# Kernel tuning notes

Hardware: AMD Instinct MI355X
Metric: run time of the kernel (lower is better)

## Reference

```python
import jax, jax.numpy as jnp
from jax import lax
import numpy as np

B, N, C = 16, 4096, 81          # batch, rois, classes (incl. background)
VARIANCES = np.array([0.1, 0.1, 0.2, 0.2], dtype=np.float32)
MAX_TOTAL = 200                  # max_total_size (= per-class cap here)
K = 200                          # per-class candidates kept before NMS
SCORE_TH = 0.5
IOU_TH = 0.5                     # tf combined NMS default
EPS = 1e-8


def setup_inputs() -> dict:
    key = jax.random.key(0)
    k1, k2, k3, k4 = jax.random.split(key, 4)
    yx = jax.random.uniform(k1, (B, N, 2)) * 0.8
    hw = 0.05 + jax.random.uniform(k2, (B, N, 2)) * 0.15
    roi_bboxes = jnp.concatenate([yx, yx + hw], axis=-1)          # [B,N,4] y1x1y2x2 in [0,1]
    pred_deltas = jax.random.normal(k3, (B, N, C * 4)) * 0.5      # [B,N,C*4]
    logits = jax.random.normal(k4, (B, N, C)) * 3.0
    pred_label_probs = jax.nn.softmax(logits, axis=-1)            # [B,N,C]
    return {"roi_bboxes": roi_bboxes, "pred_deltas": pred_deltas,
            "pred_label_probs": pred_label_probs}


def delta_to_bbox(anchors, deltas):
    # anchors [...,4] y1,x1,y2,x2 ; deltas [...,4] dy,dx,dh,dw
    ah = anchors[..., 2] - anchors[..., 0]
    aw = anchors[..., 3] - anchors[..., 1]
    acy = anchors[..., 0] + 0.5 * ah
    acx = anchors[..., 1] + 0.5 * aw
    bh = jnp.exp(deltas[..., 2]) * ah
    bw = jnp.exp(deltas[..., 3]) * aw
    bcy = deltas[..., 0] * ah + acy
    bcx = deltas[..., 1] * aw + acx
    y1 = bcy - 0.5 * bh
    x1 = bcx - 0.5 * bw
    return jnp.stack([y1, x1, y1 + bh, x1 + bw], axis=-1)


def pairwise_iou(boxes):  # [K,4] -> [K,K]
    y1 = jnp.maximum(boxes[:, None, 0], boxes[None, :, 0])
    x1 = jnp.maximum(boxes[:, None, 1], boxes[None, :, 1])
    y2 = jnp.minimum(boxes[:, None, 2], boxes[None, :, 2])
    x2 = jnp.minimum(boxes[:, None, 3], boxes[None, :, 3])
    inter = jnp.maximum(y2 - y1, 0.0) * jnp.maximum(x2 - x1, 0.0)
    area = jnp.maximum(boxes[:, 2] - boxes[:, 0], 0.0) * jnp.maximum(boxes[:, 3] - boxes[:, 1], 0.0)
    union = area[:, None] + area[None, :] - inter
    return inter / (union + EPS)


def _nms_keep(boxes_k, scores_k):
    # boxes_k [K,4] sorted by score desc; greedy suppression mask
    ious = pairwise_iou(boxes_k)
    rng = jnp.arange(K)
    valid = scores_k > SCORE_TH

    def step(keep, i):
        sup = (ious[i] > IOU_TH) & (rng > i) & keep[i]
        return keep & ~sup, None

    keep, _ = lax.scan(step, valid, rng)
    return keep


def _per_class(boxes_c, scores_c):
    # boxes_c [N,4], scores_c [N] -> top-K candidates + NMS-kept scores
    sc, idx = lax.top_k(scores_c, K)
    bx = boxes_c[idx]                       # [K,4]
    keep = _nms_keep(bx, sc)
    return bx, jnp.where(keep, sc, 0.0)


def _per_image(boxes_b, scores_b):
    # boxes_b [N,C,4], scores_b [N,C]
    bx, sc = jax.vmap(_per_class, in_axes=(1, 1))(boxes_b, scores_b)  # [C,K,4],[C,K]
    top_sc, top_idx = lax.top_k(sc.reshape(-1), MAX_TOTAL)
    top_bx = bx.reshape(-1, 4)[top_idx]
    top_lbl = (top_idx // K).astype(jnp.float32)
    valid = top_sc > 0.0
    top_bx = jnp.clip(jnp.where(valid[:, None], top_bx, 0.0), 0.0, 1.0)  # clip_boxes=True
    return top_bx, jnp.where(valid, top_sc, 0.0), jnp.where(valid, top_lbl, 0.0)


def reference(roi_bboxes, pred_deltas, pred_label_probs):
    b, n, _ = roi_bboxes.shape
    c = pred_label_probs.shape[-1]
    deltas = pred_deltas.reshape(b, n, c, 4) * jnp.asarray(VARIANCES)
    pred_bboxes = delta_to_bbox(roi_bboxes[:, :, None, :], deltas)       # [B,N,C,4]
    bg = jnp.argmax(pred_label_probs, axis=-1) == 0                      # background mask
    scores = jnp.where(bg[..., None], 0.0, pred_label_probs)             # [B,N,C]
    final_bboxes, final_scores, final_labels = jax.vmap(_per_image)(pred_bboxes, scores)
    return final_bboxes, final_labels, final_scores
```

## Files before the change

### kernel.cpp

```cpp
#include <hip/hip_runtime.h>
#include <math.h>

#pragma clang fp contract(off)

constexpr int NB  = 16;
constexpr int NR  = 4096;
constexpr int NC  = 81;
constexpr int NCM1 = NC - 1;
constexpr int KK  = 200;
constexpr int CAP = 4096;
constexpr int MAXC = 1024;
constexpr int TCHUNK = 256;
constexpr int NCHUNK = CAP / TCHUNK;
constexpr float SCORE_TH = 0.5f;
constexpr float IOU_TH   = 0.5f;
constexpr float EPSF     = 1e-8f;

struct SK { float s; int key; };

__global__ void k_perclass(const float* __restrict__ probs,
                           const float* __restrict__ roi,
                           const float* __restrict__ deltas,
                           int* __restrict__ kcnt,
                           SK* __restrict__ sk_seg,
                           float4* __restrict__ fbox_seg) {
    __shared__ int   lcnt;
    __shared__ float ls[MAXC], lroi[MAXC];
    __shared__ float ss[KK], sy1[KK], sx1[KK], sy2[KK], sx2[KK], sar[KK];
    __shared__ unsigned long long sup[KK][4];
    __shared__ int   skeep[KK];

    const int bid = blockIdx.x, tid = threadIdx.x;
    const int b = bid / NCM1, cm1 = bid % NCM1, c = cm1 + 1;

    if (tid == 0) lcnt = 0;
    __syncthreads();

    const float* pcol = probs + (size_t)b * NR * NC + c;
    #pragma unroll 4
    for (int r = tid; r < NR; r += 256) {
        float p = pcol[(size_t)r * NC];
        if (p > SCORE_TH) {
            int q = atomicAdd(&lcnt, 1);
            if (q < MAXC) { ls[q] = p; lroi[q] = (float)r; }
        }
    }
    __syncthreads();

    int Mc = lcnt < MAXC ? lcnt : MAXC;
    if (Mc == 0) {
        if (tid == 0) kcnt[b * NCM1 + cm1] = 0;
        return;
    }

    for (int i = tid; i < Mc; i += 256) {
        float si = ls[i], ri = lroi[i];
        int rank = 0;
        for (int j = 0; j < Mc; ++j) {
            float sj = ls[j], rj = lroi[j];
            rank += (int)((sj > si) | ((sj == si) & (rj < ri)));
        }
        if (rank < KK) {
            int r = (int)ri;
            float4 a = ((const float4*)roi)[(size_t)b * NR + r];
            float4 d = *(const float4*)(deltas + (((size_t)b * NR + r) * NC + c) * 4);
            float ah  = a.z - a.x;
            float aw  = a.w - a.y;
            float acy = a.x + 0.5f * ah;
            float acx = a.y + 0.5f * aw;
            float dy = d.x * 0.1f, dx = d.y * 0.1f;
            float dh = d.z * 0.2f, dw = d.w * 0.2f;
            float bh  = expf(dh) * ah;
            float bw  = expf(dw) * aw;
            float bcy = dy * ah + acy;
            float bcx = dx * aw + acx;
            float y1 = bcy - 0.5f * bh;
            float x1 = bcx - 0.5f * bw;
            float y2 = y1 + bh;
            float x2 = x1 + bw;
            ss[rank] = si;
            sy1[rank] = y1; sx1[rank] = x1; sy2[rank] = y2; sx2[rank] = x2;
            sar[rank] = fmaxf(y2 - y1, 0.f) * fmaxf(x2 - x1, 0.f);
        }
    }
    __syncthreads();

    int L = Mc < KK ? Mc : KK;

    for (int idx = tid; idx < L * 4; idx += 256) {
        int i = idx >> 2, w = idx & 3;
        int j0 = w * 64;
        unsigned long long bits = 0;
        int jend = j0 + 64 < L ? j0 + 64 : L;
        int jstart = j0 > i + 1 ? j0 : i + 1;
        if (jstart < jend) {
            float yi1 = sy1[i], xi1 = sx1[i], yi2 = sy2[i], xi2 = sx2[i], ai = sar[i];
            for (int j = jstart; j < jend; ++j) {
                float yy1 = fmaxf(yi1, sy1[j]), xx1 = fmaxf(xi1, sx1[j]);
                float yy2 = fminf(yi2, sy2[j]), xx2 = fminf(xi2, sx2[j]);
                float inter = fmaxf(yy2 - yy1, 0.f) * fmaxf(xx2 - xx1, 0.f);
                float uni = ai + sar[j] - inter;
                if (inter / (uni + EPSF) > IOU_TH) bits |= 1ull << (j - j0);
            }
        }
        sup[i][w] = bits;
    }
    __syncthreads();

    if (tid < 64) {
        int lane = tid;
        int kmask = 0;
        #pragma unroll
        for (int s = 0; s < 4; ++s) if (s * 64 + lane < L) kmask |= 1 << s;
        for (int i = 0; i < L; ++i) {
            int oi = i & 63, si = i >> 6;
            unsigned long long r0 = sup[i][0], r1 = sup[i][1];
            unsigned long long r2 = sup[i][2], r3 = sup[i][3];
            int keep_i = (__shfl(kmask, oi) >> si) & 1;
            if (keep_i) {
                int supb = (int)((r0 >> lane) & 1)
                         | ((int)((r1 >> lane) & 1) << 1)
                         | ((int)((r2 >> lane) & 1) << 2)
                         | ((int)((r3 >> lane) & 1) << 3);
                kmask &= ~supb;
            }
        }
        #pragma unroll
        for (int s = 0; s < 4; ++s) {
            int jj = s * 64 + lane;
            if (jj < L) skeep[jj] = (kmask >> s) & 1;
        }
    }
    __syncthreads();

    for (int i = tid; i < L; i += 256) {
        if (skeep[i]) {
            int pos = 0;
            for (int j = 0; j < i; ++j) pos += skeep[j];
            size_t idx = ((size_t)b * NC + c) * KK + pos;
            sk_seg[idx].s = ss[i];
            sk_seg[idx].key = c * KK + i;
            fbox_seg[idx] = make_float4(sy1[i], sx1[i], sy2[i], sx2[i]);
        }
    }
    if (tid == 0) {
        int tot = 0;
        for (int i = 0; i < L; ++i) tot += skeep[i];
        kcnt[b * NCM1 + cm1] = tot;
    }
}

__global__ void k_topk(const int* __restrict__ kcnt,
                       const SK* __restrict__ sk_seg,
                       const float4* __restrict__ fbox_seg,
                       float* __restrict__ out) {
    int b = blockIdx.x / NCHUNK, chunk = blockIdx.x % NCHUNK;
    const int tid = threadIdx.x;

    __shared__ int pfx[NCM1 + 1];
    __shared__ SK  sL[CAP];

    if (tid < NCM1) pfx[tid + 1] = kcnt[b * NCM1 + tid];
    if (tid == 0) pfx[0] = 0;
    __syncthreads();
    if (tid == 0) {
        int run = 0;
        for (int s = 1; s <= NCM1; ++s) { run += pfx[s]; pfx[s] = run; }
    }
    __syncthreads();
    int M = pfx[NCM1];

    float* obox = out + (size_t)b * KK * 4;
    float* olbl = out + (size_t)NB * KK * 4 + (size_t)b * KK;
    float* osc  = out + (size_t)NB * KK * 5 + (size_t)b * KK;

    if (chunk == 0) {
        int Mi = M < KK ? M : KK;
        for (int i = Mi + tid; i < KK; i += 256) {
            obox[i * 4 + 0] = 0.f; obox[i * 4 + 1] = 0.f;
            obox[i * 4 + 2] = 0.f; obox[i * 4 + 3] = 0.f;
            olbl[i] = 0.f; osc[i] = 0.f;
        }
    }
    if (chunk * TCHUNK >= M) return;

    for (int i = tid; i < M; i += 256) {
        int lo = 0, hi = NCM1;
        while (lo + 1 < hi + 1) {
            int mid = (lo + hi + 1) >> 1;
            if (pfx[mid] <= i) lo = mid; else hi = mid - 1;
        }
        int cseg = lo + 1;
        int k = i - pfx[lo];
        sL[i] = sk_seg[((size_t)b * NC + cseg) * KK + k];
    }
    __syncthreads();

    int e = chunk * TCHUNK + tid;
    if (e >= M) return;
    float se = sL[e].s; int ke = sL[e].key;
    int rank = 0;
    const float4* p4 = (const float4*)sL;
    int npair = M >> 1;
    #pragma unroll 4
    for (int p = 0; p < npair; ++p) {
        float4 v = p4[p];
        int k0 = __float_as_int(v.y), k1 = __float_as_int(v.w);
        rank += (int)((v.x > se) | ((v.x == se) & (k0 < ke)));
        rank += (int)((v.z > se) | ((v.z == se) & (k1 < ke)));
    }
    if (M & 1) {
        float sj = sL[M - 1].s; int kj = sL[M - 1].key;
        rank += (int)((sj > se) | ((sj == se) & (kj < ke)));
    }
    if (rank < KK) {
        float4 bx = fbox_seg[(size_t)b * NC * KK + ke];
        obox[rank * 4 + 0] = fminf(fmaxf(bx.x, 0.f), 1.f);
        obox[rank * 4 + 1] = fminf(fmaxf(bx.y, 0.f), 1.f);
        obox[rank * 4 + 2] = fminf(fmaxf(bx.z, 0.f), 1.f);
        obox[rank * 4 + 3] = fminf(fmaxf(bx.w, 0.f), 1.f);
        olbl[rank] = (float)(ke / KK);
        osc[rank]  = se;
    }
}

extern "C" void kernel_launch(void* const* d_in, const int* in_sizes, int n_in,
                              void* d_out, int out_size, void* d_ws, size_t ws_size,
                              hipStream_t stream) {
    const float* roi    = (const float*)d_in[0];
    const float* deltas = (const float*)d_in[1];
    const float* probs  = (const float*)d_in[2];
    float* out = (float*)d_out;

    char* base = (char*)d_ws;
    int*    kcnt     = (int*)base;
    SK*     sk_seg   = (SK*)(base + 8192);
    float4* fbox_seg = (float4*)(base + 8192 + 2073600);

    k_perclass<<<NB * NCM1, 256, 0, stream>>>(probs, roi, deltas,
                                              kcnt, sk_seg, fbox_seg);
    k_topk<<<NB * NCHUNK, 256, 0, stream>>>(kcnt, sk_seg, fbox_seg, out);
}
```

Before: 82.12 us.

## Fuse per-class filtering into one block per image with wave-level NMS

Replaces the per-(image,class) kernel with one 1024-thread block per image. The block stages probabilities in shared memory, computes the per-roi argmax and background mask, and then assigns each class to a wavefront that compacts candidates with ballots, ranks them, and runs greedy NMS entirely in registers via shuffles. This is meant to remove repeated strided column reads of the probability tensor and the shared-memory suppression matrix. In exchange, only 16 blocks run, which limits memory parallelism across the GPU. The workspace layout and topk indexing are adjusted to the new per-class segment layout.

```diff
diff --git a/kernel.cpp b/kernel.cpp
--- a/kernel.cpp
+++ b/kernel.cpp
@@ -9,7 +9,7 @@
 constexpr int NCM1 = NC - 1;
 constexpr int KK  = 200;
 constexpr int CAP = 4096;
-constexpr int MAXC = 1024;
+constexpr int WCAP = 256;
 constexpr int TCHUNK = 256;
 constexpr int NCHUNK = CAP / TCHUNK;
 constexpr float SCORE_TH = 0.5f;
@@ -18,135 +18,166 @@
 
 struct SK { float s; int key; };
 
-__global__ void k_perclass(const float* __restrict__ probs,
-                           const float* __restrict__ roi,
-                           const float* __restrict__ deltas,
-                           int* __restrict__ kcnt,
-                           SK* __restrict__ sk_seg,
-                           float4* __restrict__ fbox_seg) {
-    __shared__ int   lcnt;
-    __shared__ float ls[MAXC], lroi[MAXC];
-    __shared__ float ss[KK], sy1[KK], sx1[KK], sy2[KK], sx2[KK], sar[KK];
-    __shared__ unsigned long long sup[KK][4];
-    __shared__ int   skeep[KK];
-
-    const int bid = blockIdx.x, tid = threadIdx.x;
-    const int b = bid / NCM1, cm1 = bid % NCM1, c = cm1 + 1;
-
-    if (tid == 0) lcnt = 0;
-    __syncthreads();
-
-    const float* pcol = probs + (size_t)b * NR * NC + c;
-    #pragma unroll 4
-    for (int r = tid; r < NR; r += 256) {
-        float p = pcol[(size_t)r * NC];
-        if (p > SCORE_TH) {
-            int q = atomicAdd(&lcnt, 1);
-            if (q < MAXC) { ls[q] = p; lroi[q] = (float)r; }
-        }
-    }
-    __syncthreads();
-
-    int Mc = lcnt < MAXC ? lcnt : MAXC;
-    if (Mc == 0) {
-        if (tid == 0) kcnt[b * NCM1 + cm1] = 0;
-        return;
-    }
-
-    for (int i = tid; i < Mc; i += 256) {
-        float si = ls[i], ri = lroi[i];
-        int rank = 0;
-        for (int j = 0; j < Mc; ++j) {
-            float sj = ls[j], rj = lroi[j];
-            rank += (int)((sj > si) | ((sj == si) & (rj < ri)));
-        }
-        if (rank < KK) {
-            int r = (int)ri;
-            float4 a = ((const float4*)roi)[(size_t)b * NR + r];
-            float4 d = *(const float4*)(deltas + (((size_t)b * NR + r) * NC + c) * 4);
-            float ah  = a.z - a.x;
-            float aw  = a.w - a.y;
-            float acy = a.x + 0.5f * ah;
-            float acx = a.y + 0.5f * aw;
-            float dy = d.x * 0.1f, dx = d.y * 0.1f;
-            float dh = d.z * 0.2f, dw = d.w * 0.2f;
-            float bh  = expf(dh) * ah;
-            float bw  = expf(dw) * aw;
-            float bcy = dy * ah + acy;
-            float bcx = dx * aw + acx;
-            float y1 = bcy - 0.5f * bh;
-            float x1 = bcx - 0.5f * bw;
-            float y2 = y1 + bh;
-            float x2 = x1 + bw;
-            ss[rank] = si;
-            sy1[rank] = y1; sx1[rank] = x1; sy2[rank] = y2; sx2[rank] = x2;
-            sar[rank] = fmaxf(y2 - y1, 0.f) * fmaxf(x2 - x1, 0.f);
-        }
-    }
-    __syncthreads();
-
-    int L = Mc < KK ? Mc : KK;
-
-    for (int idx = tid; idx < L * 4; idx += 256) {
-        int i = idx >> 2, w = idx & 3;
-        int j0 = w * 64;
-        unsigned long long bits = 0;
-        int jend = j0 + 64 < L ? j0 + 64 : L;
-        int jstart = j0 > i + 1 ? j0 : i + 1;
-        if (jstart < jend) {
-            float yi1 = sy1[i], xi1 = sx1[i], yi2 = sy2[i], xi2 = sx2[i], ai = sar[i];
-            for (int j = jstart; j < jend; ++j) {
-                float yy1 = fmaxf(yi1, sy1[j]), xx1 = fmaxf(xi1, sx1[j]);
-                float yy2 = fminf(yi2, sy2[j]), xx2 = fminf(xi2, sx2[j]);
-                float inter = fmaxf(yy2 - yy1, 0.f) * fmaxf(xx2 - xx1, 0.f);
-                float uni = ai + sar[j] - inter;
-                if (inter / (uni + EPSF) > IOU_TH) bits |= 1ull << (j - j0);
-            }
-        }
-        sup[i][w] = bits;
-    }
-    __syncthreads();
-
-    if (tid < 64) {
-        int lane = tid;
+__device__ __forceinline__ void decode_box(const float4& a, const float4& d,
+                                           float& y1, float& x1, float& y2, float& x2) {
+    float ah  = a.z - a.x;
+    float aw  = a.w - a.y;
+    float acy = a.x + 0.5f * ah;
+    float acx = a.y + 0.5f * aw;
+    float dy = d.x * 0.1f, dx = d.y * 0.1f;
+    float dh = d.z * 0.2f, dw = d.w * 0.2f;
+    float bh  = expf(dh) * ah;
+    float bw  = expf(dw) * aw;
+    float bcy = dy * ah + acy;
+    float bcx = dx * aw + acx;
+    y1 = bcy - 0.5f * bh;
+    x1 = bcx - 0.5f * bw;
+    y2 = y1 + bh;
+    x2 = x1 + bw;
+}
+
+__global__ __launch_bounds__(1024)
+void k_fused(const float* __restrict__ roi,
+             const float* __restrict__ deltas,
+             const float* __restrict__ probs,
+             int* __restrict__ kcnt,
+             SK* __restrict__ sk_seg,
+             float4* __restrict__ fbox_seg) {
+    __shared__ float4 stage4[256 * NC / 4];
+    __shared__ float  pscore[NR];
+    __shared__ int    pcls[NR];
+
+    const int b = blockIdx.x, tid = threadIdx.x;
+    const int lane = tid & 63, w = tid >> 6;
+    const unsigned long long lmask_lt = (1ull << lane) - 1ull;
+
+    for (int t = 0; t < 16; ++t) {
+        __syncthreads();
+        const float4* src = (const float4*)(probs + ((size_t)b * NR + t * 256) * NC);
+        for (int v = tid; v < 256 * NC / 4; v += 1024) stage4[v] = src[v];
+        __syncthreads();
+        int g = tid >> 2, j = tid & 3;
+        const float* row = (const float*)stage4 + g * NC;
+        float m = -1.0f;
+        int am = 127;
+        for (int c = j; c < NC; c += 4) {
+            float v = row[c];
+            if (v > m) { m = v; am = c; }
+        }
+        for (int mask = 1; mask <= 2; mask <<= 1) {
+            float om = __shfl_xor(m, mask);
+            int   oi = __shfl_xor(am, mask);
+            if (om > m || (om == m && oi < am)) { m = om; am = oi; }
+        }
+        if (j == 0) {
+            int r = t * 256 + g;
+            pscore[r] = m;
+            pcls[r] = (am != 0 && m > SCORE_TH) ? am : 0;
+        }
+    }
+    __syncthreads();
+
+    float2* wcand = (float2*)stage4 + (size_t)w * WCAP;
+    float2* wrank = (float2*)stage4 + 16 * WCAP + (size_t)w * WCAP;
+
+    for (int cc = 0; cc < 5; ++cc) {
+        int cm1 = w + cc * 16;
+        int c = cm1 + 1;
+        int outbase = b * NCM1 + cm1;
+
+        int cnt = 0;
+        for (int base = 0; base < NR; base += 64) {
+            int r = base + lane;
+            bool pred = (pcls[r] == c);
+            unsigned long long bal = __ballot(pred);
+            if (pred) {
+                int pos = cnt + __popcll(bal & lmask_lt);
+                if (pos < WCAP) wcand[pos] = make_float2(pscore[r], (float)r);
+            }
+            cnt += __popcll(bal);
+        }
+        int Mc = cnt < WCAP ? cnt : WCAP;
+        if (Mc == 0) {
+            if (lane == 0) kcnt[outbase] = 0;
+            continue;
+        }
+        int L = Mc < KK ? Mc : KK;
+
+        #pragma unroll
+        for (int s = 0; s < 4; ++s) {
+            int i = s * 64 + lane;
+            if (i < Mc) {
+                float2 me = wcand[i];
+                int rank = 0;
+                for (int jj = 0; jj < Mc; ++jj) {
+                    float2 v = wcand[jj];
+                    rank += (int)((v.x > me.x) | ((v.x == me.x) & (v.y < me.y)));
+                }
+                if (rank < KK) wrank[rank] = me;
+            }
+        }
+
+        float bsc[4], by1[4], bx1[4], by2[4], bx2[4], bar_[4];
         int kmask = 0;
         #pragma unroll
-        for (int s = 0; s < 4; ++s) if (s * 64 + lane < L) kmask |= 1 << s;
-        for (int i = 0; i < L; ++i) {
-            int oi = i & 63, si = i >> 6;
-            unsigned long long r0 = sup[i][0], r1 = sup[i][1];
-            unsigned long long r2 = sup[i][2], r3 = sup[i][3];
-            int keep_i = (__shfl(kmask, oi) >> si) & 1;
-            if (keep_i) {
-                int supb = (int)((r0 >> lane) & 1)
-                         | ((int)((r1 >> lane) & 1) << 1)
-                         | ((int)((r2 >> lane) & 1) << 2)
-                         | ((int)((r3 >> lane) & 1) << 3);
-                kmask &= ~supb;
-            }
-        }
-        #pragma unroll
-        for (int s = 0; s < 4; ++s) {
-            int jj = s * 64 + lane;
-            if (jj < L) skeep[jj] = (kmask >> s) & 1;
-        }
-    }
-    __syncthreads();
-
-    for (int i = tid; i < L; i += 256) {
-        if (skeep[i]) {
-            int pos = 0;
-            for (int j = 0; j < i; ++j) pos += skeep[j];
-            size_t idx = ((size_t)b * NC + c) * KK + pos;
-            sk_seg[idx].s = ss[i];
-            sk_seg[idx].key = c * KK + i;
-            fbox_seg[idx] = make_float4(sy1[i], sx1[i], sy2[i], sx2[i]);
-        }
-    }
-    if (tid == 0) {
-        int tot = 0;
-        for (int i = 0; i < L; ++i) tot += skeep[i];
-        kcnt[b * NCM1 + cm1] = tot;
+        for (int s = 0; s < 4; ++s) {
+            int rho = s * 64 + lane;
+            if (rho < L) {
+                float2 me = wrank[rho];
+                int r = (int)me.y;
+                float4 a = ((const float4*)roi)[(size_t)b * NR + r];
+                float4 d = *(const float4*)(deltas + (((size_t)b * NR + r) * NC + c) * 4);
+                float y1, x1, y2, x2;
+                decode_box(a, d, y1, x1, y2, x2);
+                bsc[s] = me.x;
+                by1[s] = y1; bx1[s] = x1; by2[s] = y2; bx2[s] = x2;
+                bar_[s] = fmaxf(y2 - y1, 0.f) * fmaxf(x2 - x1, 0.f);
+                kmask |= 1 << s;
+            }
+        }
+
+        #pragma unroll
+        for (int si = 0; si < 4; ++si) {
+            int iend = (si + 1) * 64 < L ? (si + 1) * 64 : L;
+            for (int i = si * 64; i < iend; ++i) {
+                int oi = i & 63;
+                int keep_i = (__shfl(kmask, oi) >> si) & 1;
+                if (!keep_i) continue;
+                float yi1 = __shfl(by1[si], oi), xi1 = __shfl(bx1[si], oi);
+                float yi2 = __shfl(by2[si], oi), xi2 = __shfl(bx2[si], oi);
+                float ai  = __shfl(bar_[si], oi);
+                #pragma unroll
+                for (int s = 0; s < 4; ++s) {
+                    int jj = s * 64 + lane;
+                    if (jj > i && ((kmask >> s) & 1)) {
+                        float yy1 = fmaxf(yi1, by1[s]), xx1 = fmaxf(xi1, bx1[s]);
+                        float yy2 = fminf(yi2, by2[s]), xx2 = fminf(xi2, bx2[s]);
+                        float inter = fmaxf(yy2 - yy1, 0.f) * fmaxf(xx2 - xx1, 0.f);
+                        float uni = ai + bar_[s] - inter;
+                        if (inter / (uni + EPSF) > IOU_TH) kmask &= ~(1 << s);
+                    }
+                }
+            }
+        }
+
+        int tot = 0, mypos[4];
+        #pragma unroll
+        for (int s = 0; s < 4; ++s) {
+            unsigned long long bal = __ballot((kmask >> s) & 1);
+            mypos[s] = tot + __popcll(bal & lmask_lt);
+            tot += __popcll(bal);
+        }
+        size_t sb = (size_t)outbase * KK;
+        #pragma unroll
+        for (int s = 0; s < 4; ++s) {
+            int rho = s * 64 + lane;
+            if ((kmask >> s) & 1) {
+                sk_seg[sb + mypos[s]].s = bsc[s];
+                sk_seg[sb + mypos[s]].key = c * KK + rho;
+                fbox_seg[sb + rho] = make_float4(by1[s], bx1[s], by2[s], bx2[s]);
+            }
+        }
+        if (lane == 0) kcnt[outbase] = tot;
     }
 }
 
@@ -185,14 +216,13 @@
     if (chunk * TCHUNK >= M) return;
 
     for (int i = tid; i < M; i += 256) {
-        int lo = 0, hi = NCM1;
-        while (lo + 1 < hi + 1) {
+        int lo = 0, hi = NCM1 - 1;
+        while (lo < hi) {
             int mid = (lo + hi + 1) >> 1;
             if (pfx[mid] <= i) lo = mid; else hi = mid - 1;
         }
-        int cseg = lo + 1;
         int k = i - pfx[lo];
-        sL[i] = sk_seg[((size_t)b * NC + cseg) * KK + k];
+        sL[i] = sk_seg[((size_t)b * NCM1 + lo) * KK + k];
     }
     __syncthreads();
 
@@ -214,7 +244,8 @@
         rank += (int)((sj > se) | ((sj == se) & (kj < ke)));
     }
     if (rank < KK) {
-        float4 bx = fbox_seg[(size_t)b * NC * KK + ke];
+        int cm1 = ke / KK - 1, ipre = ke % KK;
+        float4 bx = fbox_seg[((size_t)b * NCM1 + cm1) * KK + ipre];
         obox[rank * 4 + 0] = fminf(fmaxf(bx.x, 0.f), 1.f);
         obox[rank * 4 + 1] = fminf(fmaxf(bx.y, 0.f), 1.f);
         obox[rank * 4 + 2] = fminf(fmaxf(bx.z, 0.f), 1.f);
@@ -234,10 +265,9 @@
 
     char* base = (char*)d_ws;
     int*    kcnt     = (int*)base;
-    SK*     sk_seg   = (SK*)(base + 8192);
-    float4* fbox_seg = (float4*)(base + 8192 + 2073600);
-
-    k_perclass<<<NB * NCM1, 256, 0, stream>>>(probs, roi, deltas,
-                                              kcnt, sk_seg, fbox_seg);
+    SK*     sk_seg   = (SK*)(base + 16384);
+    float4* fbox_seg = (float4*)(base + 16384 + 2097152);
+
+    k_fused<<<NB, 1024, 0, stream>>>(roi, deltas, probs, kcnt, sk_seg, fbox_seg);
     k_topk<<<NB * NCHUNK, 256, 0, stream>>>(kcnt, sk_seg, fbox_seg, out);
 }
```

Result: slower. 158.0 us (+92.3%).
